# Kernel optimization log

Measured on AMD Instinct MI355X. Metric: run time of the kernel, lower is better.

The kernel has to match this reference:

```python
import jax, jax.numpy as jnp
import numpy as np

# Dims (see shape_source)
B, C_IN, H, W = 32, 256, 56, 56
O, J = 256, 64            # out_channels, in_connects (sparse in-channel subset per out channel)
KH, KW = 3, 3
STRIDE = (1, 1)
PAD = (1, 1)


def setup_inputs() -> dict:
    key = jax.random.key(0)
    k1, k2 = jax.random.split(key)
    x = jax.random.normal(k1, (B, C_IN, H, W), dtype=jnp.float32)
    # init_rand_indices: each out channel samples in_connects distinct in-channels
    rng = np.random.default_rng(0)
    w_idx = jnp.asarray(
        np.stack([rng.permutation(C_IN)[:J] for _ in range(O)]), dtype=jnp.int32
    )  # [O, J]
    # reset_parameters: uniform(-stdv, +stdv), stdv = 1/sqrt(in_connects * kh * kw)
    stdv = 1.0 / np.sqrt(J * KH * KW)
    w_vals = jax.random.uniform(k2, (O, J, KH, KW), dtype=jnp.float32,
                                minval=-stdv, maxval=stdv)
    return {"x": x, "w_vals": w_vals, "w_idx": w_idx}


def reference(x, w_vals, w_idx):
    # Sparse conv: out[b,o] = sum_j conv(x[:, w_idx[o,j]], w_vals[o,j]).
    # Equivalent math: scatter sparse weights into a dense [O, C_in, KH, KW]
    # kernel (zeros on unselected channels) and run one dense conv.
    dense_w = jnp.zeros((O, C_IN, KH, KW), dtype=w_vals.dtype)
    dense_w = dense_w.at[jnp.arange(O)[:, None], w_idx].set(w_vals)
    out = jax.lax.conv_general_dilated(
        x, dense_w,
        window_strides=STRIDE,
        padding=[(PAD[0], PAD[0]), (PAD[1], PAD[1])],
        dimension_numbers=("NCHW", "OIHW", "NCHW"),
    )  # [B, O, H, W]
    return out
```

## Files before the change

### kernel.cpp

```cpp
#include <hip/hip_runtime.h>
#include <hip/hip_bf16.h>


typedef __attribute__((ext_vector_type(8))) short bf16x8;
typedef __attribute__((ext_vector_type(4))) float f32x4;

#define WD_BYTES 1179648
#define XP_BYTES 55115776
#define WS_NEED  (WD_BYTES + XP_BYTES)
#define ABUF 32768
#define BBUF 28672
#define BOFF 65536
#define LDS_TOT 122880

__global__ __launch_bounds__(256) void preproc(
    const float* __restrict__ x, const float* __restrict__ wv,
    const int* __restrict__ widx, __hip_bfloat16* __restrict__ wd,
    __hip_bfloat16* __restrict__ xp)
{
    int bid = blockIdx.x;
    int tid = threadIdx.x;
    if (bid >= 1792) {
        int o = bid - 1792;
        int j = tid & 63;
        if (tid < 64) {
#pragma unroll
            for (int k = 0; k < 9; ++k)
                reinterpret_cast<float2*>(wd + (size_t)k * 65536 + o * 256)[j] =
                    float2{0.f, 0.f};
        }
        __syncthreads();
        if (tid < 64) {
            int cin = widx[o * 64 + j];
            const float* src = wv + (size_t)(o * 64 + j) * 9;
#pragma unroll
            for (int k = 0; k < 9; ++k)
                wd[(size_t)k * 65536 + o * 256 + cin] = __float2bfloat16(src[k]);
        }
        return;
    }
    int b = bid / 56, h = bid - (bid / 56) * 56;
    __shared__ __hip_bfloat16 tile[56][264];
    int c = tid;
    const float* src = x + ((size_t)(b * 256 + c)) * 3136 + h * 56;
    float vals[56];
#pragma unroll
    for (int i = 0; i < 14; ++i) {
        float4 v = *reinterpret_cast<const float4*>(src + i * 4);
        vals[i*4+0] = v.x; vals[i*4+1] = v.y; vals[i*4+2] = v.z; vals[i*4+3] = v.w;
    }
#pragma unroll
    for (int w = 0; w < 56; ++w) tile[w][c] = __float2bfloat16(vals[w]);

    char* rowb = (char*)xp + (((size_t)b * 58 + (h + 1)) * 58) * 512;
    if (tid < 64)        reinterpret_cast<double*>(rowb)[tid] = 0.0;
    else if (tid < 128)  *reinterpret_cast<double*>(rowb + 57 * 512 + (tid - 64) * 8) = 0.0;
    if (h == 0) {
        char* r0 = (char*)xp + (((size_t)b * 58 + 0) * 58) * 512;
        for (int i = tid; i < 58 * 64; i += 256) reinterpret_cast<double*>(r0)[i] = 0.0;
    }
    if (h == 55) {
        char* r57 = (char*)xp + (((size_t)b * 58 + 57) * 58) * 512;
        for (int i = tid; i < 58 * 64; i += 256) reinterpret_cast<double*>(r57)[i] = 0.0;
    }

    __syncthreads();
    char* obase = (char*)xp + (((size_t)b * 58 + (h + 1)) * 58) * 512;
#pragma unroll
    for (int k = 0; k < 7; ++k) {
        int i = tid + k * 256;
        int w = i >> 5, cc = i & 31;
        bf16x8 v = *reinterpret_cast<const bf16x8*>(&tile[w][cc * 8]);
        *reinterpret_cast<bf16x8*>(obase + (size_t)(w + 1) * 512 + cc * 16) = v;
    }
}


__device__ __forceinline__ void gload_lds16(const void* g, void* l) {
    __builtin_amdgcn_global_load_lds(
        (const __attribute__((address_space(1))) void*)g,
        (__attribute__((address_space(3))) void*)l, 16, 0, 0);
}

template<int BB, int J>
__device__ __forceinline__ void stage_a(const char* wdB, char* smem, int wid,
                                        int sa_off, int aoff) {
    gload_lds16(wdB + aoff + J * 64 * 512 + sa_off,
                smem + BB * ABUF + (J * 64 + wid * 8) * 128);
}

template<int BB, int J>
__device__ __forceinline__ void stage_b(const char* xpB, char* smem, int wid,
                                        int pbJ, int boff) {
    gload_lds16(xpB + pbJ + boff,
                smem + BOFF + BB * BBUF + (J * 64 + wid * 8) * 128);
}

__device__ __forceinline__ int pixoff(int p) {
    int b = p / 3136; int r = p - b * 3136;
    int h = r / 56;   int w = r - h * 56;
    return ((b * 58 + h + 1) * 58 + (w + 1)) * 512;
}

__device__ __forceinline__ int aoff_t(int t) {
    return (t >> 2) * 131072 + (t & 3) * 128;
}
__device__ __forceinline__ int boff_t(int t) {
    int k9 = t >> 2; int kh = k9 / 3; int kw = k9 - 3 * kh;
    return ((kh - 1) * 58 + (kw - 1)) * 512 + (t & 3) * 128;
}

#define BAR() __builtin_amdgcn_s_barrier()
#define VMCNT0() asm volatile("s_waitcnt vmcnt(0)" ::: "memory")

template<int U>
__device__ __forceinline__ void ktile(
    const char* wdB, const char* xpB, char* smem,
    int wid, int wr, int wc, int a_rb, int xq0, int xq1, int sa_off,
    int pb0, int pb1, int pb2, int pb3,
    int tn, f32x4 (&acc)[4][7])
{
    const int an = aoff_t(tn), bn = boff_t(tn);
    stage_a<1-U,0>(wdB, smem, wid, sa_off, an);
    stage_a<1-U,1>(wdB, smem, wid, sa_off, an);
    stage_a<1-U,2>(wdB, smem, wid, sa_off, an);
    stage_a<1-U,3>(wdB, smem, wid, sa_off, an);
    stage_b<1-U,0>(xpB, smem, wid, pb0, bn);
    stage_b<1-U,1>(xpB, smem, wid, pb1, bn);
    stage_b<1-U,2>(xpB, smem, wid, pb2, bn);
    if (wid < 4) stage_b<1-U,3>(xpB, smem, wid, pb3, bn);

    const int aBase = U * ABUF + wr * 64 * 128 + a_rb;
    const int bBase = BOFF + U * BBUF + wc * 112 * 128 + a_rb;

    bf16x8 af[4][2], bf[7][2];
#pragma unroll
    for (int mi = 0; mi < 4; ++mi) {
        af[mi][0] = *(const bf16x8*)(smem + aBase + mi * 16 * 128 + xq0);
        af[mi][1] = *(const bf16x8*)(smem + aBase + mi * 16 * 128 + xq1);
    }
#pragma unroll
    for (int ni = 0; ni < 7; ++ni) {
        bf[ni][0] = *(const bf16x8*)(smem + bBase + ni * 16 * 128 + xq0);
        bf[ni][1] = *(const bf16x8*)(smem + bBase + ni * 16 * 128 + xq1);
    }
    __builtin_amdgcn_s_setprio(1);
#pragma unroll
    for (int mi = 0; mi < 4; ++mi)
#pragma unroll
        for (int ni = 0; ni < 7; ++ni)
#pragma unroll
            for (int s = 0; s < 2; ++s)
                acc[mi][ni] = __builtin_amdgcn_mfma_f32_16x16x32_bf16(
                    af[mi][s], bf[ni][s], acc[mi][ni], 0, 0, 0);
    __builtin_amdgcn_s_setprio(0);

    VMCNT0();
    BAR();
}

__global__ __launch_bounds__(512, 2) void sparse_conv_mfma224(
    const __hip_bfloat16* __restrict__ wd, const __hip_bfloat16* __restrict__ xp,
    float* __restrict__ out)
{
    extern __shared__ char smem[];
    const char* wdB = (const char*)wd;
    const char* xpB = (const char*)xp;

    const int nt = blockIdx.x;
    const int t = threadIdx.x;
    const int lane = t & 63, wid = t >> 6;
    const int wr = wid >> 1, wc = wid & 1;

    const int axor = (((lane & 7) ^ (lane >> 3)) * 16);
    const int sa_off = (wid * 8 + (lane >> 3)) * 512 + axor;
    const int prow = wid * 8 + (lane >> 3);
    const int pb0 = pixoff(nt * 224 +   0 + prow) + axor;
    const int pb1 = pixoff(nt * 224 +  64 + prow) + axor;
    const int pb2 = pixoff(nt * 224 + 128 + prow) + axor;
    const int pb3 = (wid < 4) ? (pixoff(nt * 224 + 192 + prow) + axor) : 0;

    const int a_rb = (lane & 15) * 128;
    const int xq0 = (((lane >> 4)) ^ (lane & 7)) * 16;
    const int xq1 = ((4 + (lane >> 4)) ^ (lane & 7)) * 16;

    f32x4 acc[4][7] = {};

    {
        const int a0 = aoff_t(0), b0 = boff_t(0);
        stage_a<0,0>(wdB, smem, wid, sa_off, a0);
        stage_a<0,1>(wdB, smem, wid, sa_off, a0);
        stage_a<0,2>(wdB, smem, wid, sa_off, a0);
        stage_a<0,3>(wdB, smem, wid, sa_off, a0);
        stage_b<0,0>(xpB, smem, wid, pb0, b0);
        stage_b<0,1>(xpB, smem, wid, pb1, b0);
        stage_b<0,2>(xpB, smem, wid, pb2, b0);
        if (wid < 4) stage_b<0,3>(xpB, smem, wid, pb3, b0);
        VMCNT0();
        BAR();
    }

    for (int it = 0; it < 18; ++it) {
        const int t1 = 2 * it + 1;
        int t2 = t1 + 1; if (t2 == 36) t2 = 0;
        ktile<0>(wdB, xpB, smem, wid, wr, wc, a_rb, xq0, xq1, sa_off,
                 pb0, pb1, pb2, pb3, t1, acc);
        ktile<1>(wdB, xpB, smem, wid, wr, wc, a_rb, xq0, xq1, sa_off,
                 pb0, pb1, pb2, pb3, t2, acc);
    }

#pragma unroll
    for (int n = 0; n < 7; ++n) {
        int p0 = nt * 224 + wc * 112 + n * 16;
        int pb = p0 / 3136;
        int rem0 = p0 - pb * 3136;
#pragma unroll
        for (int m = 0; m < 4; ++m) {
            int o = wr * 64 + m * 16 + (lane >> 4) * 4;
            float* dst = out + ((size_t)(pb * 256 + o)) * 3136 + rem0 + (lane & 15);
#pragma unroll
            for (int r = 0; r < 4; ++r) dst[(size_t)r * 3136] = acc[m][n][r];
        }
    }
}


__global__ __launch_bounds__(256) void sparse_conv_direct(
    const float* __restrict__ x, const float* __restrict__ wv,
    const int* __restrict__ widx, float* __restrict__ out)
{
    const int bid = blockIdx.x;
    const int b = bid >> 8, o = bid & 255;
    const int tid = threadIdx.x;
    __shared__ float plane[58 * 60];
    const int rt = tid >> 3, ct = tid & 7;
    const int r0 = rt * 2, c0 = ct * 7;
    const bool active = (rt < 28);
    float acc[2][7];
#pragma unroll
    for (int i = 0; i < 2; ++i)
#pragma unroll
        for (int c = 0; c < 7; ++c) acc[i][c] = 0.f;
    const float* xb = x + (size_t)b * 256 * 3136;
    const int* idxp = widx + o * 64;
    const float* wp0 = wv + (size_t)o * 64 * 9;
    for (int j = 0; j < 64; ++j) {
        const int cin = idxp[j];
        const float* src = xb + cin * 3136;
        __syncthreads();
        for (int i = tid; i < 58 * 58; i += 256) {
            const int r = i / 58, c = i - r * 58;
            const int h = r - 1, w = c - 1;
            float v = 0.f;
            if ((unsigned)h < 56u && (unsigned)w < 56u) v = src[h * 56 + w];
            plane[r * 60 + c] = v;
        }
        float wreg[9];
#pragma unroll
        for (int k = 0; k < 9; ++k) wreg[k] = wp0[j * 9 + k];
        __syncthreads();
        if (active) {
            float rows[4][9];
#pragma unroll
            for (int dr = 0; dr < 4; ++dr)
#pragma unroll
                for (int cc = 0; cc < 9; ++cc)
                    rows[dr][cc] = plane[(r0 + dr) * 60 + (c0 + cc)];
#pragma unroll
            for (int i = 0; i < 2; ++i)
#pragma unroll
                for (int cc = 0; cc < 7; ++cc) {
                    float s = acc[i][cc];
#pragma unroll
                    for (int kh = 0; kh < 3; ++kh)
#pragma unroll
                        for (int kw = 0; kw < 3; ++kw)
                            s += rows[i + kh][cc + kw] * wreg[kh * 3 + kw];
                    acc[i][cc] = s;
                }
        }
    }
    if (active) {
        float* op = out + (size_t)bid * 3136;
#pragma unroll
        for (int i = 0; i < 2; ++i)
#pragma unroll
            for (int cc = 0; cc < 7; ++cc)
                op[(r0 + i) * 56 + (c0 + cc)] = acc[i][cc];
    }
}

extern "C" void kernel_launch(void* const* d_in, const int* in_sizes, int n_in,
                              void* d_out, int out_size, void* d_ws, size_t ws_size,
                              hipStream_t stream) {
    const float* x    = (const float*)d_in[0];
    const float* wv   = (const float*)d_in[1];
    const int*   widx = (const int*)d_in[2];
    float* out = (float*)d_out;
    (void)in_sizes; (void)n_in; (void)out_size;

    if (ws_size < (size_t)WS_NEED) {
        sparse_conv_direct<<<dim3(32 * 256), dim3(256), 0, stream>>>(x, wv, widx, out);
        return;
    }

    __hip_bfloat16* wd = (__hip_bfloat16*)d_ws;
    __hip_bfloat16* xp = (__hip_bfloat16*)((char*)d_ws + WD_BYTES);

    preproc<<<dim3(32 * 56 + 256), dim3(256), 0, stream>>>(x, wv, widx, wd, xp);

    (void)hipFuncSetAttribute((const void*)sparse_conv_mfma224,
                              hipFuncAttributeMaxDynamicSharedMemorySize, LDS_TOT);
    sparse_conv_mfma224<<<dim3(448), dim3(512), LDS_TOT, stream>>>(wd, xp, out);
}
```

Baseline: 151.5 us.

## Issue first LDS fragment reads before global staging, split MFMA by k-half, remap blocks

Moves the LDS reads of the first k-half fragments ahead of the global-to-LDS staging loads for the next tile, so LDS latency overlaps with issuing global loads. The MFMA loop is split into two passes over k-halves, so the first pass can start while the second half's fragments are still loading. Block indices are also permuted (bid&7)*56+(bid>>3), likely to spread neighbouring tiles across XCDs and improve L2 locality. This raises register pressure and relies on the compiler keeping the intended ordering.

```diff
diff --git a/kernel.cpp b/kernel.cpp
--- a/kernel.cpp
+++ b/kernel.cpp
@@ -120,6 +120,18 @@
     int pb0, int pb1, int pb2, int pb3,
     int tn, f32x4 (&acc)[4][7])
 {
+    const int aBase = U * ABUF + wr * 64 * 128 + a_rb;
+    const int bBase = BOFF + U * BBUF + wc * 112 * 128 + a_rb;
+
+    bf16x8 af0[4], bf0[7], af1[4], bf1[7];
+    af0[0] = *(const bf16x8*)(smem + aBase + xq0);
+#pragma unroll
+    for (int ni = 0; ni < 7; ++ni)
+        bf0[ni] = *(const bf16x8*)(smem + bBase + ni * 16 * 128 + xq0);
+#pragma unroll
+    for (int mi = 1; mi < 4; ++mi)
+        af0[mi] = *(const bf16x8*)(smem + aBase + mi * 16 * 128 + xq0);
+
     const int an = aoff_t(tn), bn = boff_t(tn);
     stage_a<1-U,0>(wdB, smem, wid, sa_off, an);
     stage_a<1-U,1>(wdB, smem, wid, sa_off, an);
@@ -130,29 +142,27 @@
     stage_b<1-U,2>(xpB, smem, wid, pb2, bn);
     if (wid < 4) stage_b<1-U,3>(xpB, smem, wid, pb3, bn);
 
-    const int aBase = U * ABUF + wr * 64 * 128 + a_rb;
-    const int bBase = BOFF + U * BBUF + wc * 112 * 128 + a_rb;
-
-    bf16x8 af[4][2], bf[7][2];
-#pragma unroll
-    for (int mi = 0; mi < 4; ++mi) {
-        af[mi][0] = *(const bf16x8*)(smem + aBase + mi * 16 * 128 + xq0);
-        af[mi][1] = *(const bf16x8*)(smem + aBase + mi * 16 * 128 + xq1);
-    }
-#pragma unroll
-    for (int ni = 0; ni < 7; ++ni) {
-        bf[ni][0] = *(const bf16x8*)(smem + bBase + ni * 16 * 128 + xq0);
-        bf[ni][1] = *(const bf16x8*)(smem + bBase + ni * 16 * 128 + xq1);
-    }
+    af1[0] = *(const bf16x8*)(smem + aBase + xq1);
+#pragma unroll
+    for (int ni = 0; ni < 7; ++ni)
+        bf1[ni] = *(const bf16x8*)(smem + bBase + ni * 16 * 128 + xq1);
+#pragma unroll
+    for (int mi = 1; mi < 4; ++mi)
+        af1[mi] = *(const bf16x8*)(smem + aBase + mi * 16 * 128 + xq1);
+
     __builtin_amdgcn_s_setprio(1);
 #pragma unroll
     for (int mi = 0; mi < 4; ++mi)
 #pragma unroll
         for (int ni = 0; ni < 7; ++ni)
-#pragma unroll
-            for (int s = 0; s < 2; ++s)
-                acc[mi][ni] = __builtin_amdgcn_mfma_f32_16x16x32_bf16(
-                    af[mi][s], bf[ni][s], acc[mi][ni], 0, 0, 0);
+            acc[mi][ni] = __builtin_amdgcn_mfma_f32_16x16x32_bf16(
+                af0[mi], bf0[ni], acc[mi][ni], 0, 0, 0);
+#pragma unroll
+    for (int mi = 0; mi < 4; ++mi)
+#pragma unroll
+        for (int ni = 0; ni < 7; ++ni)
+            acc[mi][ni] = __builtin_amdgcn_mfma_f32_16x16x32_bf16(
+                af1[mi], bf1[ni], acc[mi][ni], 0, 0, 0);
     __builtin_amdgcn_s_setprio(0);
 
     VMCNT0();
@@ -167,7 +177,9 @@
     const char* wdB = (const char*)wd;
     const char* xpB = (const char*)xp;
 
-    const int nt = blockIdx.x;
+    const int bid = blockIdx.x;
+    const int nt = (bid & 7) * 56 + (bid >> 3);
+
     const int t = threadIdx.x;
     const int lane = t & 63, wid = t >> 6;
     const int wr = wid >> 1, wc = wid & 1;
```

Result: faster. 148.4 us (-2.1%).
